# Performance work log

Measured on AMD Instinct MI355X. Metric: run time of the kernel, lower is better.

The kernel has to match this reference:

```python
import jax, jax.numpy as jnp
import numpy as np

B, T, H, C = 1024, 1024, 128, 6  # batch, time, hidden_dim, output_dim


def setup_inputs() -> dict:
    key = jax.random.key(0)
    ks = jax.random.split(key, 16)
    xv = jax.random.normal(ks[0], (B, T, C), dtype=jnp.float32)
    m = (jax.random.uniform(ks[1], (B, T, C)) < 0.6).astype(jnp.float32)  # binary observed mask
    dt = jax.random.uniform(ks[2], (B, T, 1), dtype=jnp.float32) * 2.0    # positive time gaps
    x = jnp.concatenate([xv, m, dt], axis=-1)  # [B,T,13]
    s = 0.05
    return {
        "x": x,
        "x_mean": jnp.zeros((C,), jnp.float32),
        "decay_x_w": jnp.ones((C,), jnp.float32),
        "decay_x_b": jnp.zeros((C,), jnp.float32),
        "decay_h_w": jnp.ones((H,), jnp.float32),
        "decay_h_b": jnp.zeros((H,), jnp.float32),
        "w_ih": jax.random.normal(ks[3], (3 * H, 2 * C), jnp.float32) * s,
        "w_hh": jax.random.normal(ks[4], (3 * H, H), jnp.float32) * s,
        "b_ih": jnp.zeros((3 * H,), jnp.float32),
        "b_hh": jnp.zeros((3 * H,), jnp.float32),
        "w1": jax.random.normal(ks[5], (H, H), jnp.float32) * s,
        "b1": jnp.zeros((H,), jnp.float32),
        "w2": jax.random.normal(ks[6], (C, H), jnp.float32) * s,
        "b2": jnp.zeros((C,), jnp.float32),
        "wu1": jax.random.normal(ks[7], (H // 2, H), jnp.float32) * s,
        "bu1": jnp.zeros((H // 2,), jnp.float32),
        "wu2": jax.random.normal(ks[8], (C, H // 2), jnp.float32) * s,
        "bu2": jnp.zeros((C,), jnp.float32),
    }


def _grud_forward(x, x_mean, decay_x_w, decay_x_b, decay_h_w, decay_h_b,
                  w_ih, w_hh, b_ih, b_hh, w1, b1, w2, b2, wu1, bu1, wu2, bu2):
    xv = jnp.transpose(x[:, :, :C], (1, 0, 2))        # [T,B,C]
    m = jnp.transpose(x[:, :, C:2 * C], (1, 0, 2))    # [T,B,C]
    dt = jnp.transpose(x[:, :, 2 * C:2 * C + 1], (1, 0, 2))  # [T,B,1]

    def step(carry, inp):
        running, x_last, h = carry
        xv_t, m_t, dt_t = inp
        obs = m_t > 0.5
        running = jnp.where(obs, 0.0, running + dt_t)          # delta_t
        gamma_x = jnp.exp(-jax.nn.relu(running * decay_x_w + decay_x_b))  # [B,C]
        gamma_h = jnp.exp(-jax.nn.relu(dt_t * decay_h_w + decay_h_b))     # [B,H]
        h = gamma_h * h
        x_last = jnp.where(obs, xv_t, x_last)
        x_hat = m_t * xv_t + (1.0 - m_t) * (gamma_x * x_last + (1.0 - gamma_x) * x_mean)
        gru_in = jnp.concatenate([x_hat, m_t], axis=-1)        # [B,2C]
        gi = gru_in @ w_ih.T + b_ih                            # [B,3H]
        gh = h @ w_hh.T + b_hh                                 # [B,3H]
        i_r, i_z, i_n = jnp.split(gi, 3, axis=-1)
        h_r, h_z, h_n = jnp.split(gh, 3, axis=-1)
        r = jax.nn.sigmoid(i_r + h_r)
        z = jax.nn.sigmoid(i_z + h_z)
        n = jnp.tanh(i_n + r * h_n)
        h = (1.0 - z) * n + z * h
        pred = jax.nn.relu(h @ w1.T + b1) @ w2.T + b2
        unc = jax.nn.softplus(jax.nn.relu(h @ wu1.T + bu1) @ wu2.T + bu2)
        return (running, x_last, h), (pred, unc)

    bsz = x.shape[0]
    init = (jnp.zeros((bsz, C), x.dtype), jnp.zeros((bsz, C), x.dtype), jnp.zeros((bsz, H), x.dtype))
    _, (pred, unc) = jax.lax.scan(step, init, (xv, m, dt))
    return jnp.transpose(pred, (1, 0, 2)), jnp.transpose(unc, (1, 0, 2))


def reference(x, x_mean, decay_x_w, decay_x_b, decay_h_w, decay_h_b,
              w_ih, w_hh, b_ih, b_hh, w1, b1, w2, b2, wu1, bu1, wu2, bu2):
    return _grud_forward(x, x_mean, decay_x_w, decay_x_b, decay_h_w, decay_h_b,
                         w_ih, w_hh, b_ih, b_hh, w1, b1, w2, b2, wu1, bu1, wu2, bu2)
```

## Files before the change

kernel.cpp:

```cpp
#include <hip/hip_runtime.h>

namespace {
constexpr int NB = 1024, NT = 1024, NH = 128;
constexpr float L2E = 1.4426950408889634f;

typedef __bf16 bf16x8 __attribute__((ext_vector_type(8)));
typedef float  f32x4  __attribute__((ext_vector_type(4)));
typedef int    i32x4  __attribute__((ext_vector_type(4)));
union FRAG { i32x4 i; bf16x8 b; };

__device__ __forceinline__ unsigned short bfb(float f) {
  union { __bf16 h; unsigned short u; } c; c.h = (__bf16)f; return c.u;
}
__device__ __forceinline__ unsigned pkbf(float a, float b) {
  return (unsigned)bfb(a) | ((unsigned)bfb(b) << 16);
}
__device__ __forceinline__ unsigned long long pk4(const f32x4 v) {
  return (unsigned long long)pkbf(v[0], v[1]) |
         ((unsigned long long)pkbf(v[2], v[3]) << 32);
}
__device__ __forceinline__ float ex2(float x) { return __builtin_amdgcn_exp2f(x); }
__device__ __forceinline__ float rcp_(float x) { return __builtin_amdgcn_rcpf(x); }

__device__ __forceinline__ FRAG pk8(const float* pp, float sc) {
  FRAG f;
  #pragma unroll
  for (int j = 0; j < 4; ++j)
    f.i[j] = (int)pkbf(pp[2 * j] * sc, pp[2 * j + 1] * sc);
  return f;
}
}

#define MFMA(a, b, c) __builtin_amdgcn_mfma_f32_16x16x32_bf16(a, b, c, 0, 0, 0)
#define BAR() do { \
  asm volatile("s_waitcnt lgkmcnt(0)" ::: "memory"); \
  __builtin_amdgcn_s_barrier(); \
} while (0)

__global__ __launch_bounds__(512, 2)
void grud_combo(const float* __restrict__ x, const float* __restrict__ x_mean,
                const float* __restrict__ dxw, const float* __restrict__ dxb,
                const float* __restrict__ dhw, const float* __restrict__ dhb,
                const float* __restrict__ w_ih, const float* __restrict__ w_hh,
                const float* __restrict__ b_ih, const float* __restrict__ b_hh,
                const float* __restrict__ w1, const float* __restrict__ b1,
                const float* __restrict__ w2, const float* __restrict__ b2,
                const float* __restrict__ wu1, const float* __restrict__ bu1,
                const float* __restrict__ wu2, const float* __restrict__ bu2,
                float* __restrict__ out,
                char* __restrict__ hcur, const char* __restrict__ hprev,
                float* __restrict__ hstate, float* __restrict__ runst,
                float* __restrict__ xlst, int t0, int t0p, int Tc, int niter)
{
  __shared__ __align__(16) char lds[40960];

  const int tid = threadIdx.x;

  if (blockIdx.x < 64) {
    if (t0 >= NT) return;

    float (*xw)[16][17] = (float(*)[16][17])lds;
    unsigned short (*gin)[16][40] = (unsigned short(*)[16][40])(lds + 2176);
    char* hdL = lds + 4736;

    const int lane = tid & 63, wv = tid >> 6;
    const int lr = lane & 15, lg = lane >> 4;
    const int b0 = blockIdx.x * 16;
    const int uidx = wv * 16 + lr;
    const int uu0  = wv * 16 + 4 * lg;

    FRAG bhh[3][4], bgi[3];
    #pragma unroll
    for (int g = 0; g < 3; ++g) {
      const float sc = (g < 2) ? -L2E : 2.f * L2E;
      const int grow = g * 128 + uidx;
      const float* wrow = w_hh + (size_t)grow * NH;
      #pragma unroll
      for (int s = 0; s < 4; ++s) bhh[g][s] = pk8(wrow + 32 * s + 8 * lg, sc);
      FRAG f; f.i = i32x4{0, 0, 0, 0};
      if (lg < 2) {
        unsigned e[8];
        #pragma unroll
        for (int j = 0; j < 8; ++j) {
          const int c = 8 * lg + j; float v = 0.f;
          if (c < 12) {
            const int ch = c >> 1;
            v = ((c & 1) ? w_ih[(size_t)grow * 12 + 6 + ch]
                         : w_ih[(size_t)grow * 12 + ch]) * sc;
          } else if (c == 12) {
            v = ((g < 2) ? (b_ih[grow] + b_hh[grow]) : b_ih[grow]) * sc;
          }
          e[j] = bfb(v);
        }
        f.i[0] = (int)(e[0] | (e[1] << 16)); f.i[1] = (int)(e[2] | (e[3] << 16));
        f.i[2] = (int)(e[4] | (e[5] << 16)); f.i[3] = (int)(e[6] | (e[7] << 16));
      }
      bgi[g] = f;
    }
    f32x4 dhwV, dhbV, bhnV;
    #pragma unroll
    for (int r = 0; r < 4; ++r) {
      dhwV[r] = -L2E * dhw[uu0 + r];
      dhbV[r] = -L2E * dhb[uu0 + r];
      bhnV[r] = b_hh[256 + uu0 + r] * (2.f * L2E);
    }

    const int  item = wv * 24 + lane;
    const bool xl = (wv < 4) && (lane < 24);
    const int  xrow = item / 6, xch = item - 6 * (item / 6);
    float dxwS = 0.f, dxbS = 0.f, xm_l = 0.f, run = 0.f, xlast = 0.f;
    if (xl) {
      dxwS = -L2E * dxw[xch]; dxbS = -L2E * dxb[xch]; xm_l = x_mean[xch];
      if (t0 > 0) { run = runst[(b0 + xrow) * 6 + xch]; xlast = xlst[(b0 + xrow) * 6 + xch]; }
    }

    const bool sl = (tid >= 256) && (tid < 464);
    const int sid = tid - 256;
    const int rrow = sid / 13, rcc = sid - 13 * (sid / 13);
    const float* xbase = x + (size_t)(b0 + rrow) * (NT * 13) + rcc;

    f32x4 hn = {0.f, 0.f, 0.f, 0.f};
    if (t0 > 0) hn = *(const f32x4*)&hstate[(size_t)(b0 + lr) * NH + uu0];

    const int wOff = lr * 256 + (((2 * wv + (lg >> 1)) ^ (lr & 7)) << 4) + (lg & 1) * 8;
    int rOff[4];
    #pragma unroll
    for (int s = 0; s < 4; ++s) rOff[s] = lr * 256 + (((4 * s + lg) ^ (lr & 7)) << 4);

    for (int i = tid; i < 2 * 16 * 28; i += 512) {
      const int buf = i / 448, rem = i - 448 * buf;
      const int row = rem / 28, c = 12 + rem - 28 * (rem / 28);
      gin[buf][row][c] = (c == 12) ? (unsigned short)0x3F80 : (unsigned short)0;
    }

    const int cb0 = t0 & 1;
    if (sl) {
      xw[cb0][rrow][rcc]     = xbase[(size_t)t0 * 13];
      const int t1 = (t0 + 1 < NT) ? t0 + 1 : NT - 1;
      xw[cb0 ^ 1][rrow][rcc] = xbase[(size_t)t1 * 13];
    }
    __syncthreads();

    f32x4 hd;
    {
      const float dt0 = xw[cb0][lr][12];
      #pragma unroll
      for (int r = 0; r < 4; ++r)
        hd[r] = ex2(fminf(dt0 * dhwV[r] + dhbV[r], 0.f)) * hn[r];
      *(unsigned long long*)(hdL + cb0 * 4096 + wOff) = pk4(hd);
    }
    if (xl) {
      const float xv = xw[cb0][xrow][xch], mt = xw[cb0][xrow][6 + xch];
      const float dtv = xw[cb0][xrow][12];
      const bool obs = mt > 0.5f;
      run = obs ? 0.f : run + dtv;
      const float gx = ex2(fminf(run * dxwS + dxbS, 0.f));
      xlast = obs ? xv : xlast;
      const float xh = mt * xv + (1.f - mt) * (gx * xlast + (1.f - gx) * xm_l);
      ((unsigned*)&gin[cb0][xrow][0])[xch] = pkbf(xh, mt);
    }
    float xr2 = 0.f;
    if (sl) { const int t2 = (t0 + 2 < NT) ? t0 + 2 : NT - 1; xr2 = xbase[(size_t)t2 * 13]; }
    BAR();

    char* hwp = hcur + (((size_t)blockIdx.x * Tc) << 12) + wv * 32 + lg * 8 + lr * 256;
    const f32x4 z4 = {0.f, 0.f, 0.f, 0.f};
    const int tend = t0 + Tc;

    #pragma unroll 1
    for (int t = t0; t < tend; ++t) {
      const int p = t & 1, q = p ^ 1;

      FRAG ag; ag.i = *(const i32x4*)&gin[p][lr][8 * lg];
      FRAG ah[4];
      #pragma unroll
      for (int s = 0; s < 4; ++s)
        ah[s].i = *(const i32x4*)(hdL + p * 4096 + rOff[s]);
      const float dtn = xw[q][lr][12];

      if (sl) {
        xw[p][rrow][rcc] = xr2;
        xr2 = xbase[(size_t)((t + 3 < NT) ? t + 3 : NT - 1) * 13];
      }

      f32x4 accr = MFMA(bgi[0].b, ag.b, z4);
      f32x4 accz = MFMA(bgi[1].b, ag.b, z4);
      f32x4 ani  = MFMA(bgi[2].b, ag.b, z4);
      f32x4 anh  = z4;
      #pragma unroll
      for (int s = 0; s < 4; ++s) {
        accr = MFMA(bhh[0][s].b, ah[s].b, accr);
        accz = MFMA(bhh[1][s].b, ah[s].b, accz);
        anh  = MFMA(bhh[2][s].b, ah[s].b, anh);
      }

      f32x4 hbv = anh + bhnV;
      #pragma unroll
      for (int r = 0; r < 4; ++r) {
        const float Er = ex2(accr[r]);
        const float rr = rcp_(1.f + Er);
        const float na = __builtin_fmaf(rr, hbv[r], ani[r]);
        const float En = ex2(na);
        const float Ez = ex2(accz[r]);
        const float em1 = En - 1.f, ep1 = En + 1.f;
        const float num = __builtin_fmaf(hd[r], ep1, em1 * Ez);
        const float den = ep1 * (1.f + Ez);
        hn[r] = num * rcp_(den);
      }

      *(unsigned long long*)hwp = pk4(hn);
      hwp += 4096;

      #pragma unroll
      for (int r = 0; r < 4; ++r)
        hd[r] = ex2(fminf(dtn * dhwV[r] + dhbV[r], 0.f)) * hn[r];
      *(unsigned long long*)(hdL + q * 4096 + wOff) = pk4(hd);

      if (xl && t + 1 < tend) {
        const float xv = xw[q][xrow][xch], mt = xw[q][xrow][6 + xch];
        const float dtv = xw[q][xrow][12];
        const bool obs = mt > 0.5f;
        run = obs ? 0.f : run + dtv;
        const float gx = ex2(fminf(run * dxwS + dxbS, 0.f));
        xlast = obs ? xv : xlast;
        const float xh = mt * xv + (1.f - mt) * (gx * xlast + (1.f - gx) * xm_l);
        ((unsigned*)&gin[q][xrow][0])[xch] = pkbf(xh, mt);
      }
      BAR();
    }

    *(f32x4*)&hstate[(size_t)(b0 + lr) * NH + uu0] = hn;
    if (xl) { runst[(b0 + xrow) * 6 + xch] = run; xlst[(b0 + xrow) * 6 + xch] = xlast; }

  } else {
    if (t0p < 0) return;

    const int hb = blockIdx.x - 64;
    const int tid2 = tid & 255, half = tid >> 8;
    const int lane2 = tid2 & 63, w4 = tid2 >> 6;
    const int lr = lane2 & 15, lg = lane2 >> 4;
    char* ldsH = lds + half * 20480;

    FRAG bw1a[4], bw1b[4], bq1[4], bw2[4], bq2[2];
    #pragma unroll
    for (int s = 0; s < 4; ++s) {
      bw1a[s] = pk8(w1 + (size_t)((2 * w4) * 16 + lr) * 128 + 32 * s + 8 * lg, 1.f);
      bw1b[s] = pk8(w1 + (size_t)((2 * w4 + 1) * 16 + lr) * 128 + 32 * s + 8 * lg, 1.f);
      bq1[s]  = pk8(wu1 + (size_t)(w4 * 16 + lr) * 128 + 32 * s + 8 * lg, 1.f);
      if (lr < 6) bw2[s] = pk8(w2 + (size_t)lr * 128 + 32 * s + 8 * lg, 1.f);
      else        bw2[s].i = i32x4{0, 0, 0, 0};
      if (s < 2) {
        if (lr < 6) bq2[s] = pk8(wu2 + (size_t)lr * 64 + 32 * s + 8 * lg, 1.f);
        else        bq2[s].i = i32x4{0, 0, 0, 0};
      }
    }
    const float b1a = b1[(2 * w4) * 16 + lr], b1b = b1[(2 * w4 + 1) * 16 + lr];
    const float bu1l = bu1[w4 * 16 + lr];
    const float b2l = (lr < 6) ? b2[lr] : 0.f, bu2l = (lr < 6) ? bu2[lr] : 0.f;
    const f32x4 z4 = {0.f, 0.f, 0.f, 0.f};

    const int tc2 = Tc >> 1, total = 64 * tc2;
    const int cy0 = (2 * w4) * 16 + lr, cy1 = (2 * w4 + 1) * 16 + lr;
    const int cu = w4 * 16 + lr;

    #pragma unroll 1
    for (int it = 0; it < niter; ++it) {
      const int hu = it * 384 + hb * 2 + half;
      const bool valid = hu < total;
      int chain = 0, tp = 0;
      if (valid) { chain = hu / tc2; tp = hu - chain * tc2; }

      if (valid) {
        const char* src = hprev + (((size_t)chain * Tc + tp * 2) << 12);
        const int o = tid2 * 16, row = o >> 8, cell = (o >> 4) & 15;
        #pragma unroll
        for (int k2 = 0; k2 < 2; ++k2) {
          uint4 v = *(const uint4*)(src + k2 * 4096 + o);
          *(uint4*)(ldsH + k2 * 4096 + row * 256 + ((cell ^ (row & 7)) << 4)) = v;
        }
      }
      __syncthreads();

      if (valid) {
        #pragma unroll
        for (int k = 0; k < 2; ++k) {
          FRAG A[4];
          #pragma unroll
          for (int s = 0; s < 4; ++s)
            A[s].i = *(const i32x4*)(ldsH + k * 4096 + lr * 256 +
                                     (((4 * s + lg) ^ (lr & 7)) << 4));
          f32x4 aa = z4, ab = z4, au = z4;
          #pragma unroll
          for (int s = 0; s < 4; ++s) {
            aa = MFMA(A[s].b, bw1a[s].b, aa);
            ab = MFMA(A[s].b, bw1b[s].b, ab);
            au = MFMA(A[s].b, bq1[s].b, au);
          }
          #pragma unroll
          for (int r = 0; r < 4; ++r) {
            const int m = k * 16 + 4 * lg + r;
            *(unsigned short*)(ldsH + 8192 + m * 256 + (((cy0 >> 3) ^ (m & 7)) << 4) +
                               (cy0 & 7) * 2) = bfb(fmaxf(aa[r] + b1a, 0.f));
            *(unsigned short*)(ldsH + 8192 + m * 256 + (((cy1 >> 3) ^ (m & 7)) << 4) +
                               (cy1 & 7) * 2) = bfb(fmaxf(ab[r] + b1b, 0.f));
            *(unsigned short*)(ldsH + 16384 + m * 128 + (((cu >> 3) ^ (m & 7)) << 4) +
                               (cu & 7) * 2) = bfb(fmaxf(au[r] + bu1l, 0.f));
          }
        }
      }
      __syncthreads();

      if (valid && w4 < 2) {
        const int mrow = w4 * 16 + lr;
        FRAG Y[4], U[2];
        #pragma unroll
        for (int s = 0; s < 4; ++s)
          Y[s].i = *(const i32x4*)(ldsH + 8192 + mrow * 256 +
                                   (((4 * s + lg) ^ (lr & 7)) << 4));
        #pragma unroll
        for (int s = 0; s < 2; ++s)
          U[s].i = *(const i32x4*)(ldsH + 16384 + mrow * 128 +
                                   (((4 * s + lg) ^ (lr & 7)) << 4));
        f32x4 ap = z4, aq = z4;
        #pragma unroll
        for (int s = 0; s < 4; ++s) ap = MFMA(Y[s].b, bw2[s].b, ap);
        #pragma unroll
        for (int s = 0; s < 2; ++s) aq = MFMA(U[s].b, bq2[s].b, aq);

        if (lr < 6) {
          const int t = t0p + tp * 2 + w4;
          #pragma unroll
          for (int r = 0; r < 4; ++r) {
            const int b = chain * 16 + 4 * lg + r;
            const size_t o = ((size_t)b * NT + t) * 6 + lr;
            out[o] = ap[r] + b2l;
            const float xa = aq[r] + bu2l;
            const float sp = fmaxf(xa, 0.f) + 0.6931471805599453f *
                __builtin_amdgcn_logf(1.f + ex2(-fabsf(xa) * L2E));
            out[(size_t)NB * NT * 6 + o] = sp;
          }
        }
      }
      __syncthreads();
    }
  }
}

extern "C" void kernel_launch(void* const* d_in, const int* in_sizes, int n_in,
                              void* d_out, int out_size, void* d_ws, size_t ws_size,
                              hipStream_t stream) {
  (void)in_sizes; (void)n_in; (void)out_size;
  const float* p[18];
  for (int i = 0; i < 18; ++i) p[i] = (const float*)d_in[i];

  const size_t STATE = (size_t)1024 * 128 * 4 + 2 * (size_t)1024 * 6 * 4;
  int Tc = 256;
  while (Tc > 16 && (2 * ((size_t)Tc << 18) + STATE) > ws_size) Tc >>= 1;

  char* h0 = (char*)d_ws;
  char* h1 = h0 + ((size_t)Tc << 18);
  float* hstate = (float*)(h1 + ((size_t)Tc << 18));
  float* runst = hstate + 1024 * 128;
  float* xlst = runst + 1024 * 6;

  const int nch = NT / Tc;
  const int niter = (64 * (Tc / 2) + 383) / 384;

  for (int k = 0; k <= nch; ++k) {
    char* hcur = (k & 1) ? h1 : h0;
    const char* hprev = (k & 1) ? h0 : h1;
    hipLaunchKernelGGL(grud_combo, dim3(256), dim3(512), 0, stream,
                       p[0], p[1], p[2], p[3], p[4], p[5], p[6], p[7], p[8], p[9],
                       p[10], p[11], p[12], p[13], p[14], p[15], p[16], p[17],
                       (float*)d_out, hcur, hprev, hstate, runst, xlst,
                       k * Tc, (k - 1) * Tc, Tc, niter);
  }
}
```

Before: 879.4 us.

## Widen head grid, use all blocks in final launch, batch GRU reciprocals

The grid goes from 256 to 512 blocks, so 448 head blocks (512 in the last launch, where no recurrence runs) share the output-head work, with the stride passed as a parameter. The recurrence loop hoists the hidden-state decay exponentials ahead of the MFMAs and pairs reciprocals, so two divisions share one rcp plus multiplies. The aim is more parallelism on the off-critical-path head work and fewer transcendental ops on the serial recurrent path. Risks are co-residency pressure on the 64 recurrent blocks and slightly different rounding from the paired reciprocals.

After: 878.7 us. No clear change (-0.1%).

```diff
diff --git a/kernel.cpp b/kernel.cpp
--- a/kernel.cpp
+++ b/kernel.cpp
@@ -50,21 +50,20 @@
                 float* __restrict__ out,
                 char* __restrict__ hcur, const char* __restrict__ hprev,
                 float* __restrict__ hstate, float* __restrict__ runst,
-                float* __restrict__ xlst, int t0, int t0p, int Tc, int niter)
+                float* __restrict__ xlst, int t0, int t0p, int Tc,
+                int niter, int hb0)
 {
   __shared__ __align__(16) char lds[40960];
 
   const int tid = threadIdx.x;
-
-  if (blockIdx.x < 64) {
-    if (t0 >= NT) return;
-
+  const int lane = tid & 63, wv = tid >> 6;
+  const int lr = lane & 15, lg = lane >> 4;
+
+  if (t0 < NT && blockIdx.x < 64) {
     float (*xw)[16][17] = (float(*)[16][17])lds;
     unsigned short (*gin)[16][40] = (unsigned short(*)[16][40])(lds + 2176);
     char* hdL = lds + 4736;
 
-    const int lane = tid & 63, wv = tid >> 6;
-    const int lr = lane & 15, lg = lane >> 4;
     const int b0 = blockIdx.x * 16;
     const int uidx = wv * 16 + lr;
     const int uu0  = wv * 16 + 4 * lg;
@@ -171,12 +170,17 @@
     for (int t = t0; t < tend; ++t) {
       const int p = t & 1, q = p ^ 1;
 
+      const float dtn = xw[q][lr][12];
+      f32x4 gmn;
+      #pragma unroll
+      for (int r = 0; r < 4; ++r)
+        gmn[r] = ex2(fminf(dtn * dhwV[r] + dhbV[r], 0.f));
+
       FRAG ag; ag.i = *(const i32x4*)&gin[p][lr][8 * lg];
       FRAG ah[4];
       #pragma unroll
       for (int s = 0; s < 4; ++s)
         ah[s].i = *(const i32x4*)(hdL + p * 4096 + rOff[s]);
-      const float dtn = xw[q][lr][12];
 
       if (sl) {
         xw[p][rrow][rcc] = xr2;
@@ -195,25 +199,35 @@
       }
 
       f32x4 hbv = anh + bhnV;
+      float A[4];
+      #pragma unroll
+      for (int r = 0; r < 4; ++r) A[r] = 1.f + ex2(accr[r]);
+      const float R01 = rcp_(A[0] * A[1]);
+      const float R23 = rcp_(A[2] * A[3]);
+      float rr[4];
+      rr[0] = A[1] * R01; rr[1] = A[0] * R01;
+      rr[2] = A[3] * R23; rr[3] = A[2] * R23;
+
+      float num[4], den[4];
       #pragma unroll
       for (int r = 0; r < 4; ++r) {
-        const float Er = ex2(accr[r]);
-        const float rr = rcp_(1.f + Er);
-        const float na = __builtin_fmaf(rr, hbv[r], ani[r]);
+        const float na = __builtin_fmaf(rr[r], hbv[r], ani[r]);
         const float En = ex2(na);
         const float Ez = ex2(accz[r]);
-        const float em1 = En - 1.f, ep1 = En + 1.f;
-        const float num = __builtin_fmaf(hd[r], ep1, em1 * Ez);
-        const float den = ep1 * (1.f + Ez);
-        hn[r] = num * rcp_(den);
-      }
+        const float ep1 = En + 1.f;
+        num[r] = __builtin_fmaf(hd[r], ep1, (En - 1.f) * Ez);
+        den[r] = ep1 * (1.f + Ez);
+      }
+      const float D01 = rcp_(den[0] * den[1]);
+      const float D23 = rcp_(den[2] * den[3]);
+      hn[0] = num[0] * den[1] * D01; hn[1] = num[1] * den[0] * D01;
+      hn[2] = num[2] * den[3] * D23; hn[3] = num[3] * den[2] * D23;
 
       *(unsigned long long*)hwp = pk4(hn);
       hwp += 4096;
 
       #pragma unroll
-      for (int r = 0; r < 4; ++r)
-        hd[r] = ex2(fminf(dtn * dhwV[r] + dhbV[r], 0.f)) * hn[r];
+      for (int r = 0; r < 4; ++r) hd[r] = gmn[r] * hn[r];
       *(unsigned long long*)(hdL + q * 4096 + wOff) = pk4(hd);
 
       if (xl && t + 1 < tend) {
@@ -235,37 +249,38 @@
   } else {
     if (t0p < 0) return;
 
-    const int hb = blockIdx.x - 64;
+    const int hb = blockIdx.x - hb0;
+    const int nhb = (int)gridDim.x - hb0;
     const int tid2 = tid & 255, half = tid >> 8;
     const int lane2 = tid2 & 63, w4 = tid2 >> 6;
-    const int lr = lane2 & 15, lg = lane2 >> 4;
+    const int lr2 = lane2 & 15, lg2 = lane2 >> 4;
     char* ldsH = lds + half * 20480;
 
     FRAG bw1a[4], bw1b[4], bq1[4], bw2[4], bq2[2];
     #pragma unroll
     for (int s = 0; s < 4; ++s) {
-      bw1a[s] = pk8(w1 + (size_t)((2 * w4) * 16 + lr) * 128 + 32 * s + 8 * lg, 1.f);
-      bw1b[s] = pk8(w1 + (size_t)((2 * w4 + 1) * 16 + lr) * 128 + 32 * s + 8 * lg, 1.f);
-      bq1[s]  = pk8(wu1 + (size_t)(w4 * 16 + lr) * 128 + 32 * s + 8 * lg, 1.f);
-      if (lr < 6) bw2[s] = pk8(w2 + (size_t)lr * 128 + 32 * s + 8 * lg, 1.f);
-      else        bw2[s].i = i32x4{0, 0, 0, 0};
+      bw1a[s] = pk8(w1 + (size_t)((2 * w4) * 16 + lr2) * 128 + 32 * s + 8 * lg2, 1.f);
+      bw1b[s] = pk8(w1 + (size_t)((2 * w4 + 1) * 16 + lr2) * 128 + 32 * s + 8 * lg2, 1.f);
+      bq1[s]  = pk8(wu1 + (size_t)(w4 * 16 + lr2) * 128 + 32 * s + 8 * lg2, 1.f);
+      if (lr2 < 6) bw2[s] = pk8(w2 + (size_t)lr2 * 128 + 32 * s + 8 * lg2, 1.f);
+      else         bw2[s].i = i32x4{0, 0, 0, 0};
       if (s < 2) {
-        if (lr < 6) bq2[s] = pk8(wu2 + (size_t)lr * 64 + 32 * s + 8 * lg, 1.f);
-        else        bq2[s].i = i32x4{0, 0, 0, 0};
-      }
-    }
-    const float b1a = b1[(2 * w4) * 16 + lr], b1b = b1[(2 * w4 + 1) * 16 + lr];
-    const float bu1l = bu1[w4 * 16 + lr];
-    const float b2l = (lr < 6) ? b2[lr] : 0.f, bu2l = (lr < 6) ? bu2[lr] : 0.f;
+        if (lr2 < 6) bq2[s] = pk8(wu2 + (size_t)lr2 * 64 + 32 * s + 8 * lg2, 1.f);
+        else         bq2[s].i = i32x4{0, 0, 0, 0};
+      }
+    }
+    const float b1a = b1[(2 * w4) * 16 + lr2], b1b = b1[(2 * w4 + 1) * 16 + lr2];
+    const float bu1l = bu1[w4 * 16 + lr2];
+    const float b2l = (lr2 < 6) ? b2[lr2] : 0.f, bu2l = (lr2 < 6) ? bu2[lr2] : 0.f;
     const f32x4 z4 = {0.f, 0.f, 0.f, 0.f};
 
     const int tc2 = Tc >> 1, total = 64 * tc2;
-    const int cy0 = (2 * w4) * 16 + lr, cy1 = (2 * w4 + 1) * 16 + lr;
-    const int cu = w4 * 16 + lr;
+    const int cy0 = (2 * w4) * 16 + lr2, cy1 = (2 * w4 + 1) * 16 + lr2;
+    const int cu = w4 * 16 + lr2;
 
     #pragma unroll 1
     for (int it = 0; it < niter; ++it) {
-      const int hu = it * 384 + hb * 2 + half;
+      const int hu = it * (nhb * 2) + hb * 2 + half;
       const bool valid = hu < total;
       int chain = 0, tp = 0;
       if (valid) { chain = hu / tc2; tp = hu - chain * tc2; }
@@ -287,8 +302,8 @@
           FRAG A[4];
           #pragma unroll
           for (int s = 0; s < 4; ++s)
-            A[s].i = *(const i32x4*)(ldsH + k * 4096 + lr * 256 +
-                                     (((4 * s + lg) ^ (lr & 7)) << 4));
+            A[s].i = *(const i32x4*)(ldsH + k * 4096 + lr2 * 256 +
+                                     (((4 * s + lg2) ^ (lr2 & 7)) << 4));
           f32x4 aa = z4, ab = z4, au = z4;
           #pragma unroll
           for (int s = 0; s < 4; ++s) {
@@ -298,7 +313,7 @@
           }
           #pragma unroll
           for (int r = 0; r < 4; ++r) {
-            const int m = k * 16 + 4 * lg + r;
+            const int m = k * 16 + 4 * lg2 + r;
             *(unsigned short*)(ldsH + 8192 + m * 256 + (((cy0 >> 3) ^ (m & 7)) << 4) +
                                (cy0 & 7) * 2) = bfb(fmaxf(aa[r] + b1a, 0.f));
             *(unsigned short*)(ldsH + 8192 + m * 256 + (((cy1 >> 3) ^ (m & 7)) << 4) +
@@ -311,28 +326,28 @@
       __syncthreads();
 
       if (valid && w4 < 2) {
-        const int mrow = w4 * 16 + lr;
+        const int mrow = w4 * 16 + lr2;
         FRAG Y[4], U[2];
         #pragma unroll
         for (int s = 0; s < 4; ++s)
           Y[s].i = *(const i32x4*)(ldsH + 8192 + mrow * 256 +
-                                   (((4 * s + lg) ^ (lr & 7)) << 4));
+                                   (((4 * s + lg2) ^ (lr2 & 7)) << 4));
         #pragma unroll
         for (int s = 0; s < 2; ++s)
           U[s].i = *(const i32x4*)(ldsH + 16384 + mrow * 128 +
-                                   (((4 * s + lg) ^ (lr & 7)) << 4));
+                                   (((4 * s + lg2) ^ (lr2 & 7)) << 4));
         f32x4 ap = z4, aq = z4;
         #pragma unroll
         for (int s = 0; s < 4; ++s) ap = MFMA(Y[s].b, bw2[s].b, ap);
         #pragma unroll
         for (int s = 0; s < 2; ++s) aq = MFMA(U[s].b, bq2[s].b, aq);
 
-        if (lr < 6) {
+        if (lr2 < 6) {
           const int t = t0p + tp * 2 + w4;
           #pragma unroll
           for (int r = 0; r < 4; ++r) {
-            const int b = chain * 16 + 4 * lg + r;
-            const size_t o = ((size_t)b * NT + t) * 6 + lr;
+            const int b = chain * 16 + 4 * lg2 + r;
+            const size_t o = ((size_t)b * NT + t) * 6 + lr2;
             out[o] = ap[r] + b2l;
             const float xa = aq[r] + bu2l;
             const float sp = fmaxf(xa, 0.f) + 0.6931471805599453f *
@@ -364,15 +379,19 @@
   float* xlst = runst + 1024 * 6;
 
   const int nch = NT / Tc;
-  const int niter = (64 * (Tc / 2) + 383) / 384;
+  const int total = 64 * (Tc / 2);
 
   for (int k = 0; k <= nch; ++k) {
     char* hcur = (k & 1) ? h1 : h0;
     const char* hprev = (k & 1) ? h0 : h1;
-    hipLaunchKernelGGL(grud_combo, dim3(256), dim3(512), 0, stream,
+    const int t0 = k * Tc;
+    const int hb0 = (t0 < NT) ? 64 : 0;
+    const int stride = (512 - hb0) * 2;
+    const int niter = (total + stride - 1) / stride;
+    hipLaunchKernelGGL(grud_combo, dim3(512), dim3(512), 0, stream,
                        p[0], p[1], p[2], p[3], p[4], p[5], p[6], p[7], p[8], p[9],
                        p[10], p[11], p[12], p[13], p[14], p[15], p[16], p[17],
                        (float*)d_out, hcur, hprev, hstate, runst, xlst,
-                       k * Tc, (k - 1) * Tc, Tc, niter);
+                       t0, (k - 1) * Tc, Tc, niter, hb0);
   }
 }
```
